# Performance work log

Measured on AMD Instinct MI355X. Metric: run time of the kernel, lower is better.

## Reference

```python
import jax, jax.numpy as jnp
import numpy as np

# ---- static config (mirrors init_kwargs) ----
PILLAR_SIZE = 0.075
X_MIN, Y_MIN, Z_MIN = -54.0, -54.0, -5.0
X_MAX, Y_MAX, Z_MAX = 54.0, 54.0, 3.0
GRID_W = int(round((X_MAX - X_MIN) / PILLAR_SIZE))  # 1440
GRID_H = int(round((Y_MAX - Y_MIN) / PILLAR_SIZE))  # 1440
B = 4            # batch (lidar frames)
N = 800_000      # total points across batch
M = 120_000      # total occupied pillars across batch
C_IN = 5         # raw point features (x,y,z,intensity,timestamp)
C_GRP = 6 + C_IN # (xyz - pillar_center, xyz, pt_feature)
C_MLP = 32       # shared MLP output width
BN_EPS = 1e-3


def _pillar_centers(pillar_indices):
    """pillar_indices: (M,3) int [b, y, x] -> (M,3) float centers."""
    pi = pillar_indices.astype(jnp.float32)
    cx = (pi[:, 2] + 0.5) * PILLAR_SIZE + X_MIN
    cy = (pi[:, 1] + 0.5) * PILLAR_SIZE + Y_MIN
    cz = jnp.full_like(cx, 0.5 * (Z_MIN + Z_MAX))
    return jnp.stack([cx, cy, cz], axis=1)


def setup_inputs() -> dict:
    key = jax.random.key(0)
    ks = jax.random.split(key, 8)
    # occupied pillar cells [b, y, x]
    pil_b = jax.random.randint(ks[0], (M,), 0, B, dtype=jnp.int32)
    pil_y = jax.random.randint(ks[1], (M,), 0, GRID_H, dtype=jnp.int32)
    pil_x = jax.random.randint(ks[2], (M,), 0, GRID_W, dtype=jnp.int32)
    pillar_indices = jnp.stack([pil_b, pil_y, pil_x], axis=1)
    # each point belongs to exactly one pillar
    pillar_set_indices = jax.random.randint(ks[3], (N,), 0, M, dtype=jnp.int32)
    centers = _pillar_centers(pillar_indices)
    noise = jax.random.normal(ks[4], (N, 3), dtype=jnp.float32)
    noise = noise * jnp.array([0.3 * PILLAR_SIZE, 0.3 * PILLAR_SIZE, 1.5], jnp.float32)
    xyz = centers[pillar_set_indices] + noise  # points near their pillar center
    pt_feature = jax.random.normal(ks[5], (N, C_IN), dtype=jnp.float32)
    # shared MLP params: Linear(no bias) + BatchNorm1d(gamma, beta)
    W1 = jax.random.normal(ks[6], (C_GRP, C_MLP), dtype=jnp.float32) * np.float32(1.0 / np.sqrt(C_GRP))
    gamma1 = jnp.ones((C_MLP,), jnp.float32)
    beta1 = jnp.zeros((C_MLP,), jnp.float32)
    xyz_batch_cnt = jnp.full((B,), N // B, jnp.int32)
    return dict(xyz=xyz, pt_feature=pt_feature, W1=W1, gamma1=gamma1, beta1=beta1,
                pillar_indices=pillar_indices, pillar_set_indices=pillar_set_indices,
                xyz_batch_cnt=xyz_batch_cnt)


def reference(xyz, pt_feature, W1, gamma1, beta1, pillar_indices, pillar_set_indices, xyz_batch_cnt):
    # --- PillarQueryAndGroup: gather per-point grouped features ---
    centers = _pillar_centers(pillar_indices)            # (M, 3)
    ctr = centers[pillar_set_indices]                    # (N, 3) gather
    group_features = jnp.concatenate([xyz - ctr, xyz, pt_feature], axis=1)  # (N, 6+C)
    # --- shared MLP: Linear(no bias) -> BatchNorm1d (train-mode stats) -> ReLU ---
    h = group_features @ W1                              # (N, C_MLP)
    mean = jnp.mean(h, axis=0)
    var = jnp.var(h, axis=0)                             # biased, as torch BN uses for normalization
    h = (h - mean) * jax.lax.rsqrt(var + BN_EPS) * gamma1 + beta1
    h = jax.nn.relu(h)
    # --- scatter-max pool over pillars (CUDA scatter_max inits to 0) ---
    pooled = jax.ops.segment_max(h, pillar_set_indices, num_segments=M)
    pillar_features = jnp.maximum(pooled, 0.0)           # empty pillars -> 0; h >= 0 after ReLU
    return pillar_features                               # (M, C_MLP); dense features of SparseConvTensor
```

## Files before the change

kernel.cpp:

```cpp
#include <hip/hip_runtime.h>


#define CMLP 32
#define BN_EPS 1e-3f
#define PSIZE 0.075f
#define XMIN -54.0f
#define YMIN -54.0f
#define CZ   -1.0f
#define NREP 64
#define SCATB 4096

__device__ __forceinline__ unsigned enc_f(float x) {
  unsigned b = __float_as_uint(x);
  return (b & 0x80000000u) ? ~b : (b | 0x80000000u);
}
__device__ __forceinline__ float dec_f(unsigned u) {
  unsigned b = (u & 0x80000000u) ? (u & 0x7fffffffu) : ~u;
  return __uint_as_float(b);
}

__global__ void __launch_bounds__(256) scatter_stats_kernel(
    const float* __restrict__ xyz, const float* __restrict__ ptf,
    const float* __restrict__ W1, const float* __restrict__ gamma,
    const int* __restrict__ pil, const int* __restrict__ sidx,
    float* __restrict__ stats_rep, unsigned* __restrict__ outenc, int N) {
  const int tid = threadIdx.x;
  const int c = tid & 31;
  const float w0 = W1[0 * CMLP + c], w1 = W1[1 * CMLP + c];
  const float w2 = W1[2 * CMLP + c], w3 = W1[3 * CMLP + c];
  const float w4 = W1[4 * CMLP + c], w5 = W1[5 * CMLP + c];
  const float w6 = W1[6 * CMLP + c], w7 = W1[7 * CMLP + c];
  const float w8 = W1[8 * CMLP + c], w9 = W1[9 * CMLP + c];
  const float w10 = W1[10 * CMLP + c];
  const float sgn = (gamma[c] < 0.f) ? -1.f : 1.f;
  float s = 0.f, ss = 0.f;
  const int hw0 = (blockIdx.x * 256 + tid) >> 5;
  const int nhw = (SCATB * 256) >> 5;
  int p = hw0;
  int m = (p < N) ? sidx[p] : 0;
  while (p < N) {
    const int pn = p + nhw;
    const int mn = (pn < N) ? sidx[pn] : 0;
    float cx = fmaf((float)pil[3 * m + 2] + 0.5f, PSIZE, XMIN);
    float cy = fmaf((float)pil[3 * m + 1] + 0.5f, PSIZE, YMIN);
    float x = xyz[3 * p], y = xyz[3 * p + 1], z = xyz[3 * p + 2];
    float h = (x - cx) * w0;
    h = fmaf(y - cy, w1, h);
    h = fmaf(z - CZ, w2, h);
    h = fmaf(x, w3, h);
    h = fmaf(y, w4, h);
    h = fmaf(z, w5, h);
    h = fmaf(ptf[5 * p + 0], w6, h);
    h = fmaf(ptf[5 * p + 1], w7, h);
    h = fmaf(ptf[5 * p + 2], w8, h);
    h = fmaf(ptf[5 * p + 3], w9, h);
    h = fmaf(ptf[5 * p + 4], w10, h);
    s += h;
    ss = fmaf(h, h, ss);
    unsigned u = enc_f(sgn * h);
    unsigned* addr = &outenc[m * CMLP + c];
    if (u > *addr) atomicMax(addr, u);
    p = pn;
    m = mn;
  }
  s += __shfl_xor(s, 32);
  ss += __shfl_xor(ss, 32);
  __shared__ float red[4][64];
  const int wave = tid >> 6, lane = tid & 63;
  if (lane < 32) {
    red[wave][lane] = s;
    red[wave][32 + lane] = ss;
  }
  __syncthreads();
  if (tid < 64) {
    float v = red[0][tid] + red[1][tid] + red[2][tid] + red[3][tid];
    atomicAdd(&stats_rep[(blockIdx.x & (NREP - 1)) * 64 + tid], v);
  }
}

__global__ void finalize_kernel(const float* __restrict__ gamma,
                                const float* __restrict__ beta,
                                const float* __restrict__ stats_rep,
                                float* __restrict__ affine, float invN) {
  int c = threadIdx.x;
  if (c < CMLP) {
    float s = 0.f, ss = 0.f;
    for (int r = 0; r < NREP; r++) {
      s += stats_rep[r * 64 + c];
      ss += stats_rep[r * 64 + 32 + c];
    }
    float mean = s * invN;
    float var = ss * invN - mean * mean;
    float sc = gamma[c] * rsqrtf(var + BN_EPS);
    affine[c] = sc;
    affine[CMLP + c] = beta[c] - mean * sc;
  }
}

__global__ void __launch_bounds__(256) transform_kernel(
    unsigned* __restrict__ io, const float* __restrict__ affine, int total) {
  int i = blockIdx.x * 256 + threadIdx.x;
  if (i < total) {
    unsigned u = io[i];
    int c = i & 31;
    float v = 0.f;
    if (u) v = fmaxf(fmaf(fabsf(affine[c]), dec_f(u), affine[CMLP + c]), 0.f);
    io[i] = __float_as_uint(v);
  }
}

extern "C" void kernel_launch(void* const* d_in, const int* in_sizes, int n_in,
                              void* d_out, int out_size, void* d_ws, size_t ws_size,
                              hipStream_t stream) {
  const float* xyz = (const float*)d_in[0];
  const float* ptf = (const float*)d_in[1];
  const float* W1 = (const float*)d_in[2];
  const float* gamma = (const float*)d_in[3];
  const float* beta = (const float*)d_in[4];
  const int* pil = (const int*)d_in[5];
  const int* sidx = (const int*)d_in[6];
  unsigned* out = (unsigned*)d_out;

  int N = in_sizes[0] / 3;

  float* stats_rep = (float*)d_ws;
  float* affine = (float*)((char*)d_ws + NREP * 64 * sizeof(float));

  hipMemsetAsync(stats_rep, 0, NREP * 64 * sizeof(float), stream);
  hipMemsetAsync(out, 0, (size_t)out_size * sizeof(unsigned), stream);

  scatter_stats_kernel<<<SCATB, 256, 0, stream>>>(xyz, ptf, W1, gamma, pil,
                                                  sidx, stats_rep, out, N);
  finalize_kernel<<<1, 64, 0, stream>>>(gamma, beta, stats_rep, affine,
                                        1.0f / (float)N);
  transform_kernel<<<(out_size + 255) / 256, 256, 0, stream>>>(out, affine,
                                                               out_size);
}
```

Baseline: 171.3 us.

## Bucket per-point features into an fp16 arena, then max-pool pillars in LDS

Instead of doing global atomicMax per point and channel into the output, the first kernel appends each point's 32 features to a per-bucket arena. Each bucket covers 128 pillars and slots are handed out by an atomic cursor. Features are stored as fp16, with the pillar's local index packed into the low mantissa bit of 7 channels. A second kernel loads each bucket, applies the BN affine and ReLU, and max-reduces in shared memory before writing the output directly, which also drops the output memset and the transform pass. The trade-offs are reduced precision from fp16 and the stolen mantissa bits, points dropped once a bucket passes 1024 entries, and a large workspace; if the workspace is too small the code falls back to the old path.

```diff
diff --git a/kernel.cpp b/kernel.cpp
--- a/kernel.cpp
+++ b/kernel.cpp
@@ -1,4 +1,5 @@
 #include <hip/hip_runtime.h>
+#include <hip/hip_fp16.h>
 
 
 #define CMLP 32
@@ -9,6 +10,13 @@
 #define CZ   -1.0f
 #define NREP 64
 #define SCATB 4096
+#define SHIFT 7
+#define BCAP 1024
+
+#define OFF_STATS 0
+#define OFF_AFF   16384
+#define OFF_CUR   32768
+#define OFF_ARENA 163840
 
 __device__ __forceinline__ unsigned enc_f(float x) {
   unsigned b = __float_as_uint(x);
@@ -17,6 +25,127 @@
 __device__ __forceinline__ float dec_f(unsigned u) {
   unsigned b = (u & 0x80000000u) ? (u & 0x7fffffffu) : ~u;
   return __uint_as_float(b);
+}
+
+__global__ void __launch_bounds__(256) k1_arena(
+    const float* __restrict__ xyz, const float* __restrict__ ptf,
+    const float* __restrict__ W1, const int* __restrict__ pil,
+    const int* __restrict__ sidx, float* __restrict__ stats_rep,
+    int* __restrict__ cursors, unsigned short* __restrict__ arena, int N) {
+  const int tid = threadIdx.x;
+  const int c = tid & 31;
+  const float w0 = W1[0 * CMLP + c], w1 = W1[1 * CMLP + c];
+  const float w2 = W1[2 * CMLP + c], w3 = W1[3 * CMLP + c];
+  const float w4 = W1[4 * CMLP + c], w5 = W1[5 * CMLP + c];
+  const float w6 = W1[6 * CMLP + c], w7 = W1[7 * CMLP + c];
+  const float w8 = W1[8 * CMLP + c], w9 = W1[9 * CMLP + c];
+  const float w10 = W1[10 * CMLP + c];
+  float s = 0.f, ss = 0.f;
+  const int hw0 = (blockIdx.x * 256 + tid) >> 5;
+  const int nhw = (SCATB * 256) >> 5;
+  const bool leader = (c == 0);
+  const int src = tid & 32;
+  int p = hw0;
+  int m = (p < N) ? sidx[p] : 0;
+  int slot = 0;
+  if (p < N && leader) slot = atomicAdd(&cursors[(m >> SHIFT) * 32], 1);
+  slot = __shfl(slot, src);
+  while (p < N) {
+    const int pn = p + nhw;
+    const int mn = (pn < N) ? sidx[pn] : 0;
+    int slotn = 0;
+    if (pn < N && leader) slotn = atomicAdd(&cursors[(mn >> SHIFT) * 32], 1);
+    float cx = fmaf((float)pil[3 * m + 2] + 0.5f, PSIZE, XMIN);
+    float cy = fmaf((float)pil[3 * m + 1] + 0.5f, PSIZE, YMIN);
+    float x = xyz[3 * p], y = xyz[3 * p + 1], z = xyz[3 * p + 2];
+    float h = (x - cx) * w0;
+    h = fmaf(y - cy, w1, h);
+    h = fmaf(z - CZ, w2, h);
+    h = fmaf(x, w3, h);
+    h = fmaf(y, w4, h);
+    h = fmaf(z, w5, h);
+    h = fmaf(ptf[5 * p + 0], w6, h);
+    h = fmaf(ptf[5 * p + 1], w7, h);
+    h = fmaf(ptf[5 * p + 2], w8, h);
+    h = fmaf(ptf[5 * p + 3], w9, h);
+    h = fmaf(ptf[5 * p + 4], w10, h);
+    s += h;
+    ss = fmaf(h, h, ss);
+    unsigned short bits = __half_as_ushort(__float2half_rn(h));
+    const int local = m & ((1 << SHIFT) - 1);
+    if (c < SHIFT) bits = (unsigned short)((bits & 0xFFFEu) | ((local >> c) & 1));
+    if (slot < BCAP)
+      arena[(size_t)((m >> SHIFT) * BCAP + slot) * 32 + c] = bits;
+    slotn = __shfl(slotn, src);
+    p = pn;
+    m = mn;
+    slot = slotn;
+  }
+  s += __shfl_xor(s, 32);
+  ss += __shfl_xor(ss, 32);
+  __shared__ float red[4][64];
+  const int wave = tid >> 6, lane = tid & 63;
+  if (lane < 32) {
+    red[wave][lane] = s;
+    red[wave][32 + lane] = ss;
+  }
+  __syncthreads();
+  if (tid < 64) {
+    float v = red[0][tid] + red[1][tid] + red[2][tid] + red[3][tid];
+    atomicAdd(&stats_rep[(blockIdx.x & (NREP - 1)) * 64 + tid], v);
+  }
+}
+
+__global__ void __launch_bounds__(256) k2_pool(
+    const unsigned short* __restrict__ arena, const int* __restrict__ cursors,
+    const float* __restrict__ affine, float* __restrict__ out, int M) {
+  __shared__ float acc[128 * CMLP];
+  const int tid = threadIdx.x;
+  const int b = blockIdx.x;
+  for (int i = tid; i < 128 * CMLP; i += 256) acc[i] = 0.f;
+  const int c = tid & 31;
+  const float sc = affine[c], bi = affine[CMLP + c];
+  __syncthreads();
+  const int cnt = min(cursors[b * 32], BCAP);
+  const size_t base = (size_t)b * BCAP * 32;
+  const int hw = tid >> 5;
+  for (int kb = 0; kb < cnt; kb += 8) {
+    const int k = kb + hw;
+    const bool valid = k < cnt;
+    unsigned short raw = 0;
+    if (valid) raw = arena[base + (size_t)k * 32 + c];
+    unsigned long long mask = __ballot(raw & 1);
+    const int local = (int)((mask >> (tid & 32)) & 0x7F);
+    if (valid) {
+      float h = __half2float(__ushort_as_half(raw));
+      float v = fmaxf(fmaf(sc, h, bi), 0.f);
+      atomicMax((int*)&acc[local * CMLP + c], __float_as_int(v));
+    }
+  }
+  __syncthreads();
+  const int mbase = b << SHIFT;
+  for (int i = tid; i < 128 * CMLP; i += 256) {
+    if (mbase + (i >> 5) < M) out[(size_t)mbase * CMLP + i] = acc[i];
+  }
+}
+
+__global__ void finalize_kernel(const float* __restrict__ gamma,
+                                const float* __restrict__ beta,
+                                const float* __restrict__ stats_rep,
+                                float* __restrict__ affine, float invN) {
+  int c = threadIdx.x;
+  if (c < CMLP) {
+    float s = 0.f, ss = 0.f;
+    for (int r = 0; r < NREP; r++) {
+      s += stats_rep[r * 64 + c];
+      ss += stats_rep[r * 64 + 32 + c];
+    }
+    float mean = s * invN;
+    float var = ss * invN - mean * mean;
+    float sc = gamma[c] * rsqrtf(var + BN_EPS);
+    affine[c] = sc;
+    affine[CMLP + c] = beta[c] - mean * sc;
+  }
 }
 
 __global__ void __launch_bounds__(256) scatter_stats_kernel(
@@ -78,25 +207,6 @@
   }
 }
 
-__global__ void finalize_kernel(const float* __restrict__ gamma,
-                                const float* __restrict__ beta,
-                                const float* __restrict__ stats_rep,
-                                float* __restrict__ affine, float invN) {
-  int c = threadIdx.x;
-  if (c < CMLP) {
-    float s = 0.f, ss = 0.f;
-    for (int r = 0; r < NREP; r++) {
-      s += stats_rep[r * 64 + c];
-      ss += stats_rep[r * 64 + 32 + c];
-    }
-    float mean = s * invN;
-    float var = ss * invN - mean * mean;
-    float sc = gamma[c] * rsqrtf(var + BN_EPS);
-    affine[c] = sc;
-    affine[CMLP + c] = beta[c] - mean * sc;
-  }
-}
-
 __global__ void __launch_bounds__(256) transform_kernel(
     unsigned* __restrict__ io, const float* __restrict__ affine, int total) {
   int i = blockIdx.x * 256 + threadIdx.x;
@@ -119,20 +229,33 @@
   const float* beta = (const float*)d_in[4];
   const int* pil = (const int*)d_in[5];
   const int* sidx = (const int*)d_in[6];
-  unsigned* out = (unsigned*)d_out;
 
   int N = in_sizes[0] / 3;
-
-  float* stats_rep = (float*)d_ws;
-  float* affine = (float*)((char*)d_ws + NREP * 64 * sizeof(float));
-
-  hipMemsetAsync(stats_rep, 0, NREP * 64 * sizeof(float), stream);
-  hipMemsetAsync(out, 0, (size_t)out_size * sizeof(unsigned), stream);
-
-  scatter_stats_kernel<<<SCATB, 256, 0, stream>>>(xyz, ptf, W1, gamma, pil,
-                                                  sidx, stats_rep, out, N);
-  finalize_kernel<<<1, 64, 0, stream>>>(gamma, beta, stats_rep, affine,
-                                        1.0f / (float)N);
-  transform_kernel<<<(out_size + 255) / 256, 256, 0, stream>>>(out, affine,
-                                                               out_size);
-}
+  int M = in_sizes[5] / 3;
+  int nbuk = (M + (1 << SHIFT) - 1) >> SHIFT;
+
+  float* stats_rep = (float*)((char*)d_ws + OFF_STATS);
+  float* affine = (float*)((char*)d_ws + OFF_AFF);
+  int* cursors = (int*)((char*)d_ws + OFF_CUR);
+  unsigned short* arena = (unsigned short*)((char*)d_ws + OFF_ARENA);
+  size_t need = (size_t)OFF_ARENA + (size_t)nbuk * BCAP * 32 * sizeof(short);
+
+  if (ws_size >= need) {
+    hipMemsetAsync(d_ws, 0, OFF_ARENA, stream);
+    k1_arena<<<SCATB, 256, 0, stream>>>(xyz, ptf, W1, pil, sidx, stats_rep,
+                                        cursors, arena, N);
+    finalize_kernel<<<1, 64, 0, stream>>>(gamma, beta, stats_rep, affine,
+                                          1.0f / (float)N);
+    k2_pool<<<nbuk, 256, 0, stream>>>(arena, cursors, affine, (float*)d_out, M);
+  } else {
+    unsigned* out = (unsigned*)d_out;
+    hipMemsetAsync(stats_rep, 0, NREP * 64 * sizeof(float), stream);
+    hipMemsetAsync(out, 0, (size_t)out_size * sizeof(unsigned), stream);
+    scatter_stats_kernel<<<SCATB, 256, 0, stream>>>(xyz, ptf, W1, gamma, pil,
+                                                    sidx, stats_rep, out, N);
+    finalize_kernel<<<1, 64, 0, stream>>>(gamma, beta, stats_rep, affine,
+                                          1.0f / (float)N);
+    transform_kernel<<<(out_size + 255) / 256, 256, 0, stream>>>(out, affine,
+                                                                 out_size);
+  }
+}
```

After: 195.4 us. +14.1%, slower.
